# Kernel tuning notes

Hardware: AMD Instinct MI355X
Metric: run time of the kernel (lower is better)

The kernel has to match this reference:

```python
import jax, jax.numpy as jnp
import numpy as np

KS = 3
N = KS * KS
LN_EPS = 1e-5


def conv2d(x, w, stride=1, pad=0):
    return jax.lax.conv_general_dilated(
        x, w, (stride, stride), [(pad, pad), (pad, pad)],
        dimension_numbers=('NCHW', 'OIHW', 'NCHW'))


def layer_norm(x, g, b):
    mu = jnp.mean(x, axis=-1, keepdims=True)
    var = jnp.mean(jnp.square(x - mu), axis=-1, keepdims=True)
    return (x - mu) * jax.lax.rsqrt(var + LN_EPS) * g + b


def l2norm(x):
    n = jnp.sqrt(jnp.sum(jnp.square(x), axis=-1, keepdims=True))
    return x / jnp.maximum(n, 1e-12)


def deform_conv(x, w_p, b_p, w_d):
    # canonical DeformConv2d (kernel 3, pad 1, stride 1, no modulation)
    B, C, H, W = x.shape
    off = conv2d(x, w_p, stride=1, pad=1) + b_p[None, :, None, None]  # [B,2N,H,W]
    xp = jnp.pad(x, ((0, 0), (0, 0), (1, 1), (1, 1)))
    Hp, Wp = H + 2, W + 2
    pn = jnp.stack(jnp.meshgrid(jnp.arange(-1, 2), jnp.arange(-1, 2), indexing='ij'), 0)
    pn = pn.reshape(2, N).astype(x.dtype)  # kernel offsets, row-major (dx,dy)
    p0x = jnp.arange(1, H + 1, dtype=x.dtype)
    p0y = jnp.arange(1, W + 1, dtype=x.dtype)
    # sampling coords, [B,H,W,N]
    px = off[:, :N].transpose(0, 2, 3, 1) + p0x[None, :, None, None] + pn[0][None, None, None, :]
    py = off[:, N:].transpose(0, 2, 3, 1) + p0y[None, None, :, None] + pn[1][None, None, None, :]
    fx = jnp.floor(px)
    fy = jnp.floor(py)
    qlx = jnp.clip(fx, 0, Hp - 1)
    qly = jnp.clip(fy, 0, Wp - 1)
    qrx = jnp.clip(fx + 1, 0, Hp - 1)
    qry = jnp.clip(fy + 1, 0, Wp - 1)
    pxc = jnp.clip(px, 0, Hp - 1)
    pyc = jnp.clip(py, 0, Wp - 1)
    g_lt = (1 + (qlx - pxc)) * (1 + (qly - pyc))
    g_rb = (1 - (qrx - pxc)) * (1 - (qry - pyc))
    g_lb = (1 + (qlx - pxc)) * (1 - (qry - pyc))
    g_rt = (1 - (qrx - pxc)) * (1 + (qly - pyc))
    xf = xp.reshape(B, C, Hp * Wp)

    def gat(ix, iy):
        idx = (ix.astype(jnp.int32) * Wp + iy.astype(jnp.int32)).reshape(B, 1, -1)
        g = jnp.take_along_axis(xf, jnp.broadcast_to(idx, (B, C, idx.shape[-1])), axis=2)
        return g.reshape(B, C, H, W, N)

    xo = (g_lt[:, None] * gat(qlx, qly) + g_rb[:, None] * gat(qrx, qry)
          + g_lb[:, None] * gat(qlx, qry) + g_rt[:, None] * gat(qrx, qly))
    # [B,C,H,W,N] -> [B,C,H*ks,W*ks] (row = h*ks+kr, col = w*ks+kc)
    xo = xo.reshape(B, C, H, W, KS, KS).transpose(0, 1, 2, 4, 3, 5).reshape(B, C, H * KS, W * KS)
    return conv2d(xo, w_d, stride=KS, pad=0)


def setup_inputs() -> dict:
    key = jax.random.key(0)
    ks = jax.random.split(key, 8)
    B, C, H, W, heads = 4, 192, 64, 64, 6
    hid = 4 * C
    return {
        'x': jax.random.normal(ks[0], (B, C, H, W), dtype=jnp.float32),
        'gamma1': jnp.ones((C,), jnp.float32),
        'beta1': jnp.zeros((C,), jnp.float32),
        'gamma2': jnp.ones((C,), jnp.float32),
        'beta2': jnp.zeros((C,), jnp.float32),
        'temperature': jnp.ones((heads, 1, 1), jnp.float32),
        'w_qkv': jax.random.normal(ks[1], (3 * C, C), jnp.float32) * 0.02,
        'w_proj': jax.random.normal(ks[2], (C, C), jnp.float32) * 0.02,
        'w_p': jax.random.normal(ks[3], (2 * N, C, KS, KS), jnp.float32) * 0.01,
        'b_p': jnp.zeros((2 * N,), jnp.float32),
        'w_d': jax.random.normal(ks[4], (C, C, KS, KS), jnp.float32) * 0.02,
        'w_fc1': jax.random.normal(ks[5], (C, hid), jnp.float32) * 0.02,
        'b_fc1': jnp.zeros((hid,), jnp.float32),
        'w_fc2': jax.random.normal(ks[6], (hid, C), jnp.float32) * 0.02,
        'b_fc2': jnp.zeros((C,), jnp.float32),
    }


def reference(x, gamma1, beta1, gamma2, beta2, temperature, w_qkv, w_proj,
              w_p, b_p, w_d, w_fc1, b_fc1, w_fc2, b_fc2):
    B, C, H, W = x.shape
    heads = temperature.shape[0]
    xs = x.reshape(B, C, H * W).transpose(0, 2, 1)  # [B,HW,C]
    shortcut = xs
    xn = layer_norm(xs, gamma1, beta1).transpose(0, 2, 1).reshape(B, C, H, W)
    # SSA: deformable-conv query + channel attention over C
    q = deform_conv(xn, w_p, b_p, w_d)
    qkv = jnp.einsum('bchw,oc->bohw', xn, w_qkv)
    k_spe, v_spe = qkv[:, C:2 * C], qkv[:, 2 * C:]

    def split(t):
        return t.reshape(B, heads, C // heads, H * W)

    qh = split(q)
    kh = l2norm(split(k_spe))
    vh = l2norm(split(v_spe))
    attn = jnp.einsum('bhcn,bhdn->bhcd', qh, kh) * temperature[None]
    attn = jax.nn.softmax(attn, axis=-1)
    out = jnp.einsum('bhcd,bhdn->bhcn', attn, vh).reshape(B, C, H, W)
    out = jnp.einsum('bchw,oc->bohw', out, w_proj)
    xs2 = shortcut + out.reshape(B, C, H * W).transpose(0, 2, 1)
    h1 = layer_norm(xs2, gamma2, beta2)
    m = jax.nn.gelu(h1 @ w_fc1 + b_fc1, approximate=False) @ w_fc2 + b_fc2
    xs3 = xs2 + m
    return xs3.transpose(0, 2, 1).reshape(B, C, H, W)
```

## Files before the change

kernel.cpp:

```cpp
#include <hip/hip_runtime.h>
#include <math.h>

typedef unsigned short u16;
typedef unsigned int u32;
typedef short s16x8 __attribute__((ext_vector_type(8)));
typedef float f32x4 __attribute__((ext_vector_type(4)));

#define AS1 __attribute__((address_space(1)))
#define AS3 __attribute__((address_space(3)))

__device__ __forceinline__ float bf2f(u16 u) {
    union { u32 i; float f; } v; v.i = ((u32)u) << 16; return v.f;
}
__device__ __forceinline__ u16 f2bf(float f) {
    union { float f; u32 i; } v; v.f = f;
    u32 r = v.i + 0x7fffu + ((v.i >> 16) & 1u);
    return (u16)(r >> 16);
}
__device__ __forceinline__ void gll16(const u16* g, u16* l) {
    __builtin_amdgcn_global_load_lds((const AS1 u32*)g, (AS3 u32*)l, 16, 0, 0);
}

__global__ void prep_kernel(const float* __restrict__ wd, const float* __restrict__ wqkv,
                            const float* __restrict__ wfc1, const float* __restrict__ wfc2,
                            const float* __restrict__ wp,
                            u16* __restrict__ wdT, u16* __restrict__ wkvT,
                            u16* __restrict__ wf1T, u16* __restrict__ wf2T,
                            u16* __restrict__ wpT)
{
    int i = blockIdx.x * 256 + threadIdx.x;
    if (i < 331776) {
        int o = i / 1728, r = i % 1728;
        int p = r / 192, c = r % 192;
        int cs = c ^ ((o & 7) << 3);
        wdT[(p * 192 + o) * 192 + cs] = f2bf(wd[(o * 192 + c) * 9 + p]);
    }
    if (i < 73728) {
        int o = i / 192, c = i % 192;
        wkvT[i] = f2bf(wqkv[(192 + o) * 192 + c]);
    }
    if (i < 147456) {
        int n = i / 192, c = i % 192;
        wf1T[i] = f2bf(wfc1[c * 768 + n]);
        int n2 = i / 768, hh = i % 768;
        wf2T[i] = f2bf(wfc2[hh * 192 + n2]);
    }
    if (i < 31104) {
        int n = i / 1728, r = i % 1728;
        int p = r / 192, c = r % 192;
        wpT[i] = f2bf(wp[(n * 192 + c) * 9 + p]);
    } else if (i < 55296) {
        wpT[i] = 0;
    }
}

__global__ __launch_bounds__(256) void ln1_kernel(const float* __restrict__ x,
                                                  const float* __restrict__ g,
                                                  const float* __restrict__ be,
                                                  u16* __restrict__ xn)
{
    __shared__ float red0[256], red1[256];
    __shared__ float mu_s[64], rs_s[64];
    __shared__ float xt[64 * 193];
    __shared__ u16 tile[64 * 194];
    int t = threadIdx.x, tl = t & 63, cg = t >> 6;
    int m0 = blockIdx.x * 64;
    int b = m0 >> 12, hw0 = m0 & 4095;
    const float* xb = x + (size_t)b * 786432 + hw0 + tl;
    float s = 0.f, s2 = 0.f;
    for (int cc = cg; cc < 192; cc += 4) {
        float v = xb[cc * 4096];
        xt[tl * 193 + cc] = v;
        s += v; s2 += v * v;
    }
    red0[t] = s; red1[t] = s2;
    __syncthreads();
    if (t < 64) {
        float a = red0[t] + red0[64 + t] + red0[128 + t] + red0[192 + t];
        float q = red1[t] + red1[64 + t] + red1[128 + t] + red1[192 + t];
        float mu = a * (1.f / 192.f);
        float var = q * (1.f / 192.f) - mu * mu;
        mu_s[t] = mu; rs_s[t] = rsqrtf(var + 1e-5f);
    }
    __syncthreads();
    float mu = mu_s[tl], rs = rs_s[tl];
    for (int cc = cg; cc < 192; cc += 4) {
        float v = (xt[tl * 193 + cc] - mu) * rs * g[cc] + be[cc];
        tile[tl * 194 + cc] = f2bf(v);
    }
    __syncthreads();
    u32* dst = (u32*)(xn + (size_t)m0 * 192);
    for (int i = t; i < 64 * 96; i += 256) {
        int r = i / 96, c2 = i % 96;
        dst[i] = *(const u32*)&tile[r * 194 + c2 * 2];
    }
}

__global__ __launch_bounds__(256) void offconv_kernel(const u16* __restrict__ xn,
                                                      const u16* __restrict__ wpT,
                                                      const float* __restrict__ bp,
                                                      float* __restrict__ off)
{
    __shared__ u16 As[64 * 200];
    __shared__ u16 Bs[32 * 200];
    int bh = blockIdx.x;
    int b = bh >> 6, h = bh & 63;
    int t = threadIdx.x;
    int lane = t & 63, wv = t >> 6;
    f32x4 acc[2];
#pragma unroll
    for (int j = 0; j < 2; j++) { acc[j][0] = 0.f; acc[j][1] = 0.f; acc[j][2] = 0.f; acc[j][3] = 0.f; }
    int r = t >> 2, cq = (t & 3) * 48;
    for (int p = 0; p < 9; p++) {
        int dh = p / 3 - 1, dw = p % 3 - 1;
        int hr = h + dh, wr = r + dw;
        bool valid = (hr >= 0) && (hr < 64) && (wr >= 0) && (wr < 64);
        const u16* src = xn + ((size_t)(b * 4096 + hr * 64 + wr)) * 192 + cq;
#pragma unroll
        for (int j = 0; j < 6; j++) {
            s16x8 v = {0, 0, 0, 0, 0, 0, 0, 0};
            if (valid) v = *(const s16x8*)(src + j * 8);
            *(s16x8*)&As[r * 200 + cq + j * 8] = v;
        }
#pragma unroll
        for (int i = 0; i < 3; i++) {
            int q = t + i * 256;
            int n = q / 24, c8 = q % 24;
            *(s16x8*)&Bs[n * 200 + c8 * 8] =
                *(const s16x8*)(wpT + n * 1728 + p * 192 + c8 * 8);
        }
        __syncthreads();
#pragma unroll
        for (int kc = 0; kc < 6; kc++) {
            s16x8 af = *(const s16x8*)&As[(wv * 16 + (lane & 15)) * 200 + kc * 32 + (lane >> 4) * 8];
            s16x8 b0 = *(const s16x8*)&Bs[(lane & 15) * 200 + kc * 32 + (lane >> 4) * 8];
            s16x8 b1 = *(const s16x8*)&Bs[(16 + (lane & 15)) * 200 + kc * 32 + (lane >> 4) * 8];
            acc[0] = __builtin_amdgcn_mfma_f32_16x16x32_bf16(af, b0, acc[0], 0, 0, 0);
            acc[1] = __builtin_amdgcn_mfma_f32_16x16x32_bf16(af, b1, acc[1], 0, 0, 0);
        }
        __syncthreads();
    }
    int col = lane & 15;
    int wbase = wv * 16 + (lane >> 4) * 4;
#pragma unroll
    for (int j = 0; j < 2; j++) {
        int n = j * 16 + col;
        if (n < 18) {
            float bb = bp[n];
#pragma unroll
            for (int rr = 0; rr < 4; rr++) {
                int w = wbase + rr;
                off[((size_t)(b * 4096 + h * 64 + w)) * 18 + n] = acc[j][rr] + bb;
            }
        }
    }
}

__global__ __launch_bounds__(512, 2) void gemm_deform(const u16* __restrict__ xn,
                                                      const float* __restrict__ off,
                                                      const u16* __restrict__ wdT,
                                                      u16* __restrict__ qt)
{
    __shared__ u16 As[64 * 200];
    __shared__ u16 Bs[192 * 192];
    __shared__ int sidx[64][9][4];
    __shared__ float swt[64][9][4];
    int t = threadIdx.x, lane = t & 63, wv = t >> 6;
    int wm = wv & 1, wn = wv >> 1;
    int m0 = blockIdx.x * 64;
    int b = m0 >> 12;
    for (int i = t; i < 576; i += 512) {
        int mi = i / 9, p = i % 9;
        int m = m0 + mi;
        int hw = m & 4095;
        int h = hw >> 6, w = hw & 63;
        float ox = off[(size_t)m * 18 + p];
        float oy = off[(size_t)m * 18 + 9 + p];
        float px = ox + (float)(h + 1) + (float)(p / 3 - 1);
        float py = oy + (float)(w + 1) + (float)(p % 3 - 1);
        float fx = floorf(px), fy = floorf(py);
        float qlx = fminf(fmaxf(fx, 0.f), 65.f);
        float qly = fminf(fmaxf(fy, 0.f), 65.f);
        float qrx = fminf(fmaxf(fx + 1.f, 0.f), 65.f);
        float qry = fminf(fmaxf(fy + 1.f, 0.f), 65.f);
        float pxc = fminf(fmaxf(px, 0.f), 65.f);
        float pyc = fminf(fmaxf(py, 0.f), 65.f);
        float gxl = 1.f + (qlx - pxc), gxr = 1.f - (qrx - pxc);
        float gyl = 1.f + (qly - pyc), gyr = 1.f - (qry - pyc);
        int xl = (int)qlx, xr = (int)qrx, yl = (int)qly, yr = (int)qry;
        int cx[4] = {xl, xr, xl, xr};
        int cy[4] = {yl, yr, yr, yl};
        float cw[4] = {gxl * gyl, gxr * gyr, gxl * gyr, gxr * gyl};
#pragma unroll
        for (int k = 0; k < 4; k++) {
            bool ok = (cx[k] >= 1) && (cx[k] <= 64) && (cy[k] >= 1) && (cy[k] <= 64);
            sidx[mi][p][k] = ok ? (b * 4096 + (cx[k] - 1) * 64 + (cy[k] - 1)) * 192 : 0;
            swt[mi][p][k] = ok ? cw[k] : 0.f;
        }
    }
    __syncthreads();
    f32x4 acc[2][3];
#pragma unroll
    for (int i = 0; i < 2; i++)
#pragma unroll
        for (int j = 0; j < 3; j++) {
            acc[i][j][0] = 0.f; acc[i][j][1] = 0.f; acc[i][j][2] = 0.f; acc[i][j][3] = 0.f;
        }
    int mi = t >> 3, ch = (t & 7) * 24;
    int orow[3], oxr[3];
#pragma unroll
    for (int j = 0; j < 3; j++) {
        int o = wn * 48 + j * 16 + (lane & 15);
        orow[j] = o * 192;
        oxr[j] = (o & 7) << 3;
    }
    int kb0 = (lane >> 4) * 8;

    {
        const u16* bsrc = wdT;
#pragma unroll
        for (int i2 = 0; i2 < 9; i2++) {
            int jc = wv + 8 * i2;
            gll16(bsrc + jc * 512 + lane * 8, Bs + jc * 512);
        }
        const int*   si = sidx[mi][0];
        const float* sw = swt[mi][0];
        s16x8 pc[4][3];
#pragma unroll
        for (int k = 0; k < 4; k++)
#pragma unroll
            for (int s = 0; s < 3; s++)
                pc[k][s] = *(const s16x8*)(xn + si[k] + ch + s * 8);
        float v[24];
#pragma unroll
        for (int j = 0; j < 24; j++) v[j] = 0.f;
#pragma unroll
        for (int k = 0; k < 4; k++) {
            float wt = sw[k];
#pragma unroll
            for (int j = 0; j < 24; j++) v[j] += wt * bf2f((u16)pc[k][j >> 3][j & 7]);
        }
#pragma unroll
        for (int s = 0; s < 3; s++) {
            s16x8 ov;
#pragma unroll
            for (int e = 0; e < 8; e++) ov[e] = (short)f2bf(v[s * 8 + e]);
            *(s16x8*)&As[mi * 200 + ch + s * 8] = ov;
        }
        asm volatile("s_waitcnt vmcnt(0)" ::: "memory");
        __syncthreads();
    }

    for (int p = 0; p < 9; p++) {
        s16x8 nc[4][3];
        if (p < 8) {
            const int* si = sidx[mi][p + 1];
#pragma unroll
            for (int k = 0; k < 4; k++)
#pragma unroll
                for (int s = 0; s < 3; s++)
                    nc[k][s] = *(const s16x8*)(xn + si[k] + ch + s * 8);
        }
#pragma unroll
        for (int kk = 0; kk < 6; kk++) {
            int kb = kk * 32 + kb0;
            s16x8 af[2], bfr[3];
#pragma unroll
            for (int i = 0; i < 2; i++)
                af[i] = *(const s16x8*)&As[(wm * 32 + i * 16 + (lane & 15)) * 200 + kb];
#pragma unroll
            for (int j = 0; j < 3; j++)
                bfr[j] = *(const s16x8*)&Bs[orow[j] + (kb ^ oxr[j])];
#pragma unroll
            for (int i = 0; i < 2; i++)
#pragma unroll
                for (int j = 0; j < 3; j++)
                    acc[i][j] = __builtin_amdgcn_mfma_f32_16x16x32_bf16(af[i], bfr[j], acc[i][j], 0, 0, 0);
        }
        if (p < 8) {
            __syncthreads();
            const u16* bsrc = wdT + (size_t)(p + 1) * 36864;
#pragma unroll
            for (int i2 = 0; i2 < 9; i2++) {
                int jc = wv + 8 * i2;
                gll16(bsrc + jc * 512 + lane * 8, Bs + jc * 512);
            }
            const float* sw = swt[mi][p + 1];
            float v[24];
#pragma unroll
            for (int j = 0; j < 24; j++) v[j] = 0.f;
#pragma unroll
            for (int k = 0; k < 4; k++) {
                float wt = sw[k];
#pragma unroll
                for (int j = 0; j < 24; j++) v[j] += wt * bf2f((u16)nc[k][j >> 3][j & 7]);
            }
#pragma unroll
            for (int s = 0; s < 3; s++) {
                s16x8 ov;
#pragma unroll
                for (int e = 0; e < 8; e++) ov[e] = (short)f2bf(v[s * 8 + e]);
                *(s16x8*)&As[mi * 200 + ch + s * 8] = ov;
            }
            asm volatile("s_waitcnt vmcnt(0)" ::: "memory");
            __syncthreads();
        }
    }
    int col = lane & 15;
#pragma unroll
    for (int i = 0; i < 2; i++)
#pragma unroll
        for (int j = 0; j < 3; j++) {
            int mm = m0 + wm * 32 + i * 16 + (lane >> 4) * 4;
            int nn = wn * 48 + j * 16 + col;
#pragma unroll
            for (int r = 0; r < 4; r++)
                qt[(size_t)(mm + r) * 192 + nn] = f2bf(acc[i][j][r]);
        }
}

template<int BM, int BN, int WM, int WN, int EP>
__global__ __launch_bounds__((BM / WM) * (BN / WN) * 64)
void gemm_bt(const u16* __restrict__ A, int lda,
             const u16* __restrict__ B, int ldb, int bstride,
             void* __restrict__ out, int ldc,
             const float* __restrict__ ex1, int K,
             const float* __restrict__ ex2,
             const float* __restrict__ exg, const float* __restrict__ exb,
             void* __restrict__ out2)
{
    constexpr int BK = 32;
    constexpr int WAVES_M = BM / WM, WAVES_N = BN / WN, NW = WAVES_M * WAVES_N;
    constexpr int TM = WM / 16, TN = WN / 16;
    constexpr int NLA = BM / 16, NLB = BN / 16;
    __shared__ u16 As[BM * BK];
    __shared__ u16 Bs[BN * BK];
    int tid = threadIdx.x;
    int lane = tid & 63, wv = tid >> 6;
    int wm = wv % WAVES_M, wn = wv / WAVES_M;
    int m0 = blockIdx.x * BM, n0 = blockIdx.y * BN;
    const u16* Bp = B + (size_t)(m0 >> 12) * bstride;
    f32x4 acc[TM][TN];
#pragma unroll
    for (int i = 0; i < TM; i++)
#pragma unroll
        for (int j = 0; j < TN; j++) {
            acc[i][j][0] = 0.f; acc[i][j][1] = 0.f; acc[i][j][2] = 0.f; acc[i][j][3] = 0.f;
        }
    int arow_l = lane >> 2;
    int acol_l = (lane & 3) * 8;
    for (int k0 = 0; k0 < K; k0 += BK) {
#pragma unroll 1
        for (int j = wv; j < NLA + NLB; j += NW) {
            if (j < NLA) {
                int row = j * 16 + arow_l;
                gll16(A + (size_t)(m0 + row) * lda + k0 + acol_l, As + j * 512);
            } else {
                int row = (j - NLA) * 16 + arow_l;
                gll16(Bp + (size_t)(n0 + row) * ldb + k0 + acol_l, Bs + (j - NLA) * 512);
            }
        }
        asm volatile("s_waitcnt vmcnt(0)" ::: "memory");
        __syncthreads();
        s16x8 af[TM], bfr[TN];
#pragma unroll
        for (int i = 0; i < TM; i++)
            af[i] = *(const s16x8*)&As[(wm * WM + i * 16 + (lane & 15)) * BK + (lane >> 4) * 8];
#pragma unroll
        for (int j = 0; j < TN; j++)
            bfr[j] = *(const s16x8*)&Bs[(wn * WN + j * 16 + (lane & 15)) * BK + (lane >> 4) * 8];
#pragma unroll
        for (int i = 0; i < TM; i++)
#pragma unroll
            for (int j = 0; j < TN; j++)
                acc[i][j] = __builtin_amdgcn_mfma_f32_16x16x32_bf16(af[i], bfr[j], acc[i][j], 0, 0, 0);
        __syncthreads();
    }
    int col = lane & 15;
    int rg = lane >> 4;
    if constexpr (EP == 2) {
        u16* o = (u16*)out;
#pragma unroll
        for (int i = 0; i < TM; i++)
#pragma unroll
            for (int j = 0; j < TN; j++) {
                int mm = m0 + wm * WM + i * 16 + rg * 4;
                int nn = n0 + wn * WN + j * 16 + col;
                float bb = ex1[nn];
#pragma unroll
                for (int r = 0; r < 4; r++) {
                    float v = acc[i][j][r] + bb;
                    o[(size_t)(mm + r) * ldc + nn] = f2bf(0.5f * v * (1.f + erff(v * 0.70710678118654752f)));
                }
            }
    } else if constexpr (EP == 4) {
        __shared__ float lnA[BM][WAVES_N];
        __shared__ float lnB[BM][WAVES_N];
        float v[TM][TN][4];
        float sr[TM][4], sq[TM][4];
#pragma unroll
        for (int i = 0; i < TM; i++)
#pragma unroll
            for (int r = 0; r < 4; r++) { sr[i][r] = 0.f; sq[i][r] = 0.f; }
#pragma unroll
        for (int i = 0; i < TM; i++) {
            int mm = m0 + wm * WM + i * 16 + rg * 4;
#pragma unroll
            for (int j = 0; j < TN; j++) {
                int nn = n0 + wn * WN + j * 16 + col;
                const float* xr = ex1 + (size_t)(mm >> 12) * 786432 + (size_t)nn * 4096 + (mm & 4095);
#pragma unroll
                for (int r = 0; r < 4; r++) {
                    float vv = acc[i][j][r] + xr[r];
                    v[i][j][r] = vv;
                    sr[i][r] += vv; sq[i][r] += vv * vv;
                }
            }
        }
#pragma unroll
        for (int i = 0; i < TM; i++)
#pragma unroll
            for (int r = 0; r < 4; r++)
#pragma unroll
                for (int sh = 1; sh < 16; sh <<= 1) {
                    sr[i][r] += __shfl_xor(sr[i][r], sh);
                    sq[i][r] += __shfl_xor(sq[i][r], sh);
                }
        if (col == 0) {
#pragma unroll
            for (int i = 0; i < TM; i++)
#pragma unroll
                for (int r = 0; r < 4; r++) {
                    int row = wm * WM + i * 16 + rg * 4 + r;
                    lnA[row][wn] = sr[i][r];
                    lnB[row][wn] = sq[i][r];
                }
        }
        __syncthreads();
        float* oxs = (float*)out;
        u16* oh = (u16*)out2;
#pragma unroll
        for (int i = 0; i < TM; i++) {
            int mm = m0 + wm * WM + i * 16 + rg * 4;
#pragma unroll
            for (int r = 0; r < 4; r++) {
                int row = wm * WM + i * 16 + rg * 4 + r;
                float tot = 0.f, tq = 0.f;
#pragma unroll
                for (int q2 = 0; q2 < WAVES_N; q2++) { tot += lnA[row][q2]; tq += lnB[row][q2]; }
                float mu = tot * (1.f / 192.f);
                float var = tq * (1.f / 192.f) - mu * mu;
                float rstd = rsqrtf(var + 1e-5f);
#pragma unroll
                for (int j = 0; j < TN; j++) {
                    int nn = n0 + wn * WN + j * 16 + col;
                    float vv = v[i][j][r];
                    oxs[(size_t)(mm + r) * ldc + nn] = vv;
                    oh[(size_t)(mm + r) * ldc + nn] = f2bf((vv - mu) * rstd * exg[nn] + exb[nn]);
                }
            }
        }
    } else if constexpr (EP == 5) {
        float* o = (float*)out;
#pragma unroll
        for (int i = 0; i < TM; i++)
#pragma unroll
            for (int j = 0; j < TN; j++) {
                int mm = m0 + wm * WM + i * 16 + rg * 4;
                int nn = n0 + wn * WN + j * 16 + col;
                float bb = ex1[nn];
                size_t obase = (size_t)(mm >> 12) * 786432 + (size_t)nn * 4096;
#pragma unroll
                for (int r = 0; r < 4; r++) {
                    float vv = acc[i][j][r] + bb + ex2[(size_t)(mm + r) * ldc + nn];
                    o[obase + ((mm + r) & 4095)] = vv;
                }
            }
    } else if constexpr (EP == 6) {
        u16* o = (u16*)out;
        float* nrm = (float*)out2;
        int bI = m0 >> 12;
#pragma unroll
        for (int j = 0; j < TN; j++) {
            float s = 0.f;
#pragma unroll
            for (int i = 0; i < TM; i++) {
                int mm = m0 + wm * WM + i * 16 + rg * 4;
                int nn = n0 + wn * WN + j * 16 + col;
#pragma unroll
                for (int r = 0; r < 4; r++) {
                    u16 hb = f2bf(acc[i][j][r]);
                    o[(size_t)(mm + r) * ldc + nn] = hb;
                    float fv = bf2f(hb);
                    s += fv * fv;
                }
            }
            s += __shfl_xor(s, 16);
            s += __shfl_xor(s, 32);
            if (rg == 0) {
                int nn = n0 + wn * WN + j * 16 + col;
                atomicAdd(&nrm[bI * 384 + nn], s);
            }
        }
    }
}

__global__ __launch_bounds__(64) void attnp_kernel(const u16* __restrict__ qt,
                                                   const u16* __restrict__ kvt,
                                                   float* __restrict__ raw)
{
    __shared__ float qT[32 * 69];
    __shared__ float kT[32 * 69];
    int ch = blockIdx.x, h = blockIdx.y, b = blockIdx.z;
    int t = threadIdx.x;
    size_t base = (size_t)(b * 4096 + ch * 64);
    for (int e = t; e < 2048; e += 64) {
        int r = e >> 5, c = e & 31;
        qT[c * 69 + r] = bf2f(qt[(base + r) * 192 + h * 32 + c]);
        kT[c * 69 + r] = bf2f(kvt[(base + r) * 384 + h * 32 + c]);
    }
    __syncthreads();
    int tc = t >> 3, td = t & 7;
    int c0 = tc * 4, d0 = td * 4;
    float acc[4][4] = {};
    for (int r = 0; r < 64; r++) {
        float qv[4], kv4[4];
#pragma unroll
        for (int u = 0; u < 4; u++) { qv[u] = qT[(c0 + u) * 69 + r]; kv4[u] = kT[(d0 + u) * 69 + r]; }
#pragma unroll
        for (int u = 0; u < 4; u++)
#pragma unroll
            for (int v = 0; v < 4; v++) acc[u][v] += qv[u] * kv4[v];
    }
    float* dst = raw + (((size_t)(b * 6 + h) * 64 + ch) * 1024);
#pragma unroll
    for (int u = 0; u < 4; u++)
#pragma unroll
        for (int v = 0; v < 4; v++)
            dst[(c0 + u) * 32 + d0 + v] = acc[u][v];
}

__global__ __launch_bounds__(1024) void softmax_kernel(const float* __restrict__ raw,
                                                       const float* __restrict__ norm2,
                                                       const float* __restrict__ temp,
                                                       float* __restrict__ att2)
{
    int h = blockIdx.x, b = blockIdx.y;
    int t = threadIdx.x;
    int c = t >> 5, d = t & 31;
    __shared__ float invk[32], invv[32];
    if (t < 32)       invk[t] = 1.f / fmaxf(sqrtf(norm2[b * 384 + h * 32 + t]), 1e-12f);
    else if (t < 64)  invv[t - 32] = 1.f / fmaxf(sqrtf(norm2[b * 384 + 192 + h * 32 + (t - 32)]), 1e-12f);
    __syncthreads();
    float T = temp[h];
    const float* pr = raw + (size_t)(b * 6 + h) * 65536 + c * 32 + d;
    float v = 0.f;
#pragma unroll
    for (int ch = 0; ch < 64; ch++) v += pr[ch * 1024];
    v *= invk[d] * T;
    float mx = v;
    for (int s = 16; s > 0; s >>= 1) mx = fmaxf(mx, __shfl_xor(mx, s, 32));
    float e = expf(v - mx);
    float sm = e;
    for (int s = 16; s > 0; s >>= 1) sm += __shfl_xor(sm, s, 32);
    att2[((size_t)(b * 6 + h) * 32 + c) * 32 + d] = (e / sm) * invv[d];
}

__global__ __launch_bounds__(192) void mb_kernel(const float* __restrict__ wproj,
                                                 const float* __restrict__ att2,
                                                 u16* __restrict__ Mb)
{
    int o2 = blockIdx.x, b = blockIdx.y, t = threadIdx.x;
    int h = t >> 5, d = t & 31;
    float s = 0.f;
#pragma unroll
    for (int c = 0; c < 32; c++)
        s += wproj[o2 * 192 + h * 32 + c] * att2[((size_t)(b * 6 + h) * 32 + c) * 32 + d];
    Mb[((size_t)b * 192 + o2) * 192 + t] = f2bf(s);
}

extern "C" void kernel_launch(void* const* d_in, const int* in_sizes, int n_in,
                              void* d_out, int out_size, void* d_ws, size_t ws_size,
                              hipStream_t stream)
{
    const float* x      = (const float*)d_in[0];
    const float* gamma1 = (const float*)d_in[1];
    const float* beta1  = (const float*)d_in[2];
    const float* gamma2 = (const float*)d_in[3];
    const float* beta2  = (const float*)d_in[4];
    const float* temp   = (const float*)d_in[5];
    const float* w_qkv  = (const float*)d_in[6];
    const float* w_proj = (const float*)d_in[7];
    const float* w_p    = (const float*)d_in[8];
    const float* b_p    = (const float*)d_in[9];
    const float* w_d    = (const float*)d_in[10];
    const float* w_fc1  = (const float*)d_in[11];
    const float* b_fc1  = (const float*)d_in[12];
    const float* w_fc2  = (const float*)d_in[13];
    const float* b_fc2  = (const float*)d_in[14];
    float* out = (float*)d_out;
    char* ws = (char*)d_ws;

    u16*   xn    = (u16*)(ws + 0);
    float* off   = (float*)(ws + 6291456);
    u16*   adef  = (u16*)(ws + 7471104);
    u16*   wpT   = adef;
    u16*   m1    = adef;
    float* araw  = (float*)(ws + 32636928);
    u16*   qt    = (u16*)(ws + 64094208);
    u16*   kvt   = (u16*)(ws + 70385664);
    float* norm2 = (float*)(ws + 82968576);
    float* att2  = (float*)(ws + 83073024);
    u16*   Mb    = (u16*)(ws + 83171328);
    float* xs2   = (float*)(ws + 83318784);
    u16*   h1    = xn;
    u16*   wdT   = (u16*)(ws + 95901696);
    u16*   wkvT  = (u16*)(ws + 96565248);
    u16*   wf1T  = (u16*)(ws + 96712704);
    u16*   wf2T  = (u16*)(ws + 97007616);

    hipMemsetAsync(norm2, 0, 6144, stream);
    prep_kernel<<<1296, 256, 0, stream>>>(w_d, w_qkv, w_fc1, w_fc2, w_p, wdT, wkvT, wf1T, wf2T, wpT);
    ln1_kernel<<<256, 256, 0, stream>>>(x, gamma1, beta1, xn);
    offconv_kernel<<<256, 256, 0, stream>>>(xn, wpT, b_p, off);
    gemm_deform<<<256, 512, 0, stream>>>(xn, off, wdT, qt);
    gemm_bt<128, 128, 64, 64, 6><<<dim3(128, 3), 256, 0, stream>>>(
        xn, 192, wkvT, 192, 0, kvt, 384, nullptr, 192, nullptr, nullptr, nullptr, norm2);
    attnp_kernel<<<dim3(64, 6, 4), 64, 0, stream>>>(qt, kvt, araw);
    softmax_kernel<<<dim3(6, 4), 1024, 0, stream>>>(araw, norm2, temp, att2);
    mb_kernel<<<dim3(192, 4), 192, 0, stream>>>(w_proj, att2, Mb);
    gemm_bt<64, 192, 32, 48, 4><<<dim3(256, 1), 512, 0, stream>>>(
        kvt + 192, 384, Mb, 192, 192 * 192, xs2, 192, x, 192, nullptr, gamma2, beta2, h1);
    gemm_bt<128, 128, 64, 64, 2><<<dim3(128, 6), 256, 0, stream>>>(
        h1, 192, wf1T, 192, 0, m1, 768, b_fc1, 192, nullptr, nullptr, nullptr, nullptr);
    gemm_bt<128, 96, 32, 48, 5><<<dim3(128, 2), 512, 0, stream>>>(
        m1, 768, wf2T, 768, 0, out, 192, b_fc2, 768, xs2, nullptr, nullptr, nullptr);
}
```

Baseline: 241.9 us.

## Fuse softmax with projection-matrix build, fold memset into prep, widen offconv and attnp loads

```diff
diff --git a/kernel.cpp b/kernel.cpp
--- a/kernel.cpp
+++ b/kernel.cpp
@@ -26,9 +26,10 @@
                             const float* __restrict__ wp,
                             u16* __restrict__ wdT, u16* __restrict__ wkvT,
                             u16* __restrict__ wf1T, u16* __restrict__ wf2T,
-                            u16* __restrict__ wpT)
+                            u16* __restrict__ wpT, float* __restrict__ norm2)
 {
     int i = blockIdx.x * 256 + threadIdx.x;
+    if (i < 1536) norm2[i] = 0.f;
     if (i < 331776) {
         int o = i / 1728, r = i % 1728;
         int p = r / 192, c = r % 192;
@@ -96,7 +97,7 @@
     }
 }
 
-__global__ __launch_bounds__(256) void offconv_kernel(const u16* __restrict__ xn,
+__global__ __launch_bounds__(512) void offconv_kernel(const u16* __restrict__ xn,
                                                       const u16* __restrict__ wpT,
                                                       const float* __restrict__ bp,
                                                       float* __restrict__ off)
@@ -107,51 +108,48 @@
     int b = bh >> 6, h = bh & 63;
     int t = threadIdx.x;
     int lane = t & 63, wv = t >> 6;
-    f32x4 acc[2];
-#pragma unroll
-    for (int j = 0; j < 2; j++) { acc[j][0] = 0.f; acc[j][1] = 0.f; acc[j][2] = 0.f; acc[j][3] = 0.f; }
-    int r = t >> 2, cq = (t & 3) * 48;
+    int wm = wv & 3, wn = wv >> 2;
+    f32x4 acc;
+    acc[0] = 0.f; acc[1] = 0.f; acc[2] = 0.f; acc[3] = 0.f;
+    int r = t >> 3, cq = (t & 7) * 24;
     for (int p = 0; p < 9; p++) {
         int dh = p / 3 - 1, dw = p % 3 - 1;
         int hr = h + dh, wr = r + dw;
         bool valid = (hr >= 0) && (hr < 64) && (wr >= 0) && (wr < 64);
         const u16* src = xn + ((size_t)(b * 4096 + hr * 64 + wr)) * 192 + cq;
 #pragma unroll
-        for (int j = 0; j < 6; j++) {
+        for (int j = 0; j < 3; j++) {
             s16x8 v = {0, 0, 0, 0, 0, 0, 0, 0};
             if (valid) v = *(const s16x8*)(src + j * 8);
             *(s16x8*)&As[r * 200 + cq + j * 8] = v;
         }
 #pragma unroll
-        for (int i = 0; i < 3; i++) {
-            int q = t + i * 256;
-            int n = q / 24, c8 = q % 24;
-            *(s16x8*)&Bs[n * 200 + c8 * 8] =
-                *(const s16x8*)(wpT + n * 1728 + p * 192 + c8 * 8);
+        for (int i = 0; i < 2; i++) {
+            int q = t + i * 512;
+            if (q < 768) {
+                int n = q / 24, c8 = q % 24;
+                *(s16x8*)&Bs[n * 200 + c8 * 8] =
+                    *(const s16x8*)(wpT + n * 1728 + p * 192 + c8 * 8);
+            }
         }
         __syncthreads();
 #pragma unroll
         for (int kc = 0; kc < 6; kc++) {
-            s16x8 af = *(const s16x8*)&As[(wv * 16 + (lane & 15)) * 200 + kc * 32 + (lane >> 4) * 8];
-            s16x8 b0 = *(const s16x8*)&Bs[(lane & 15) * 200 + kc * 32 + (lane >> 4) * 8];
-            s16x8 b1 = *(const s16x8*)&Bs[(16 + (lane & 15)) * 200 + kc * 32 + (lane >> 4) * 8];
-            acc[0] = __builtin_amdgcn_mfma_f32_16x16x32_bf16(af, b0, acc[0], 0, 0, 0);
-            acc[1] = __builtin_amdgcn_mfma_f32_16x16x32_bf16(af, b1, acc[1], 0, 0, 0);
+            s16x8 af = *(const s16x8*)&As[(wm * 16 + (lane & 15)) * 200 + kc * 32 + (lane >> 4) * 8];
+            s16x8 b0 = *(const s16x8*)&Bs[(wn * 16 + (lane & 15)) * 200 + kc * 32 + (lane >> 4) * 8];
+            acc = __builtin_amdgcn_mfma_f32_16x16x32_bf16(af, b0, acc, 0, 0, 0);
         }
         __syncthreads();
     }
     int col = lane & 15;
-    int wbase = wv * 16 + (lane >> 4) * 4;
-#pragma unroll
-    for (int j = 0; j < 2; j++) {
-        int n = j * 16 + col;
-        if (n < 18) {
-            float bb = bp[n];
-#pragma unroll
-            for (int rr = 0; rr < 4; rr++) {
-                int w = wbase + rr;
-                off[((size_t)(b * 4096 + h * 64 + w)) * 18 + n] = acc[j][rr] + bb;
-            }
+    int n = wn * 16 + col;
+    int wbase = wm * 16 + (lane >> 4) * 4;
+    if (n < 18) {
+        float bb = bp[n];
+#pragma unroll
+        for (int rr = 0; rr < 4; rr++) {
+            int w = wbase + rr;
+            off[((size_t)(b * 4096 + h * 64 + w)) * 18 + n] = acc[rr] + bb;
         }
     }
 }
@@ -514,10 +512,17 @@
     int ch = blockIdx.x, h = blockIdx.y, b = blockIdx.z;
     int t = threadIdx.x;
     size_t base = (size_t)(b * 4096 + ch * 64);
-    for (int e = t; e < 2048; e += 64) {
-        int r = e >> 5, c = e & 31;
-        qT[c * 69 + r] = bf2f(qt[(base + r) * 192 + h * 32 + c]);
-        kT[c * 69 + r] = bf2f(kvt[(base + r) * 384 + h * 32 + c]);
+#pragma unroll
+    for (int i = 0; i < 4; i++) {
+        int e = t + i * 64;
+        int r = e >> 2, c8 = (e & 3) * 8;
+        s16x8 qv = *(const s16x8*)(qt + (base + r) * 192 + h * 32 + c8);
+        s16x8 kv = *(const s16x8*)(kvt + (base + r) * 384 + h * 32 + c8);
+#pragma unroll
+        for (int j = 0; j < 8; j++) {
+            qT[(c8 + j) * 69 + r] = bf2f((u16)qv[j]);
+            kT[(c8 + j) * 69 + r] = bf2f((u16)kv[j]);
+        }
     }
     __syncthreads();
     int tc = t >> 3, td = t & 7;
@@ -540,15 +545,17 @@
             dst[(c0 + u) * 32 + d0 + v] = acc[u][v];
 }
 
-__global__ __launch_bounds__(1024) void softmax_kernel(const float* __restrict__ raw,
+__global__ __launch_bounds__(1024) void attnfin_kernel(const float* __restrict__ raw,
                                                        const float* __restrict__ norm2,
                                                        const float* __restrict__ temp,
-                                                       float* __restrict__ att2)
+                                                       const float* __restrict__ wproj,
+                                                       u16* __restrict__ Mb)
 {
     int h = blockIdx.x, b = blockIdx.y;
     int t = threadIdx.x;
     int c = t >> 5, d = t & 31;
     __shared__ float invk[32], invv[32];
+    __shared__ float attL[32][33];
     if (t < 32)       invk[t] = 1.f / fmaxf(sqrtf(norm2[b * 384 + h * 32 + t]), 1e-12f);
     else if (t < 64)  invv[t - 32] = 1.f / fmaxf(sqrtf(norm2[b * 384 + 192 + h * 32 + (t - 32)]), 1e-12f);
     __syncthreads();
@@ -563,20 +570,18 @@
     float e = expf(v - mx);
     float sm = e;
     for (int s = 16; s > 0; s >>= 1) sm += __shfl_xor(sm, s, 32);
-    att2[((size_t)(b * 6 + h) * 32 + c) * 32 + d] = (e / sm) * invv[d];
-}
-
-__global__ __launch_bounds__(192) void mb_kernel(const float* __restrict__ wproj,
-                                                 const float* __restrict__ att2,
-                                                 u16* __restrict__ Mb)
-{
-    int o2 = blockIdx.x, b = blockIdx.y, t = threadIdx.x;
-    int h = t >> 5, d = t & 31;
-    float s = 0.f;
-#pragma unroll
-    for (int c = 0; c < 32; c++)
-        s += wproj[o2 * 192 + h * 32 + c] * att2[((size_t)(b * 6 + h) * 32 + c) * 32 + d];
-    Mb[((size_t)b * 192 + o2) * 192 + t] = f2bf(s);
+    attL[c][d] = (e / sm) * invv[d];
+    __syncthreads();
+#pragma unroll
+    for (int i2 = 0; i2 < 6; i2++) {
+        int i = t + i2 * 1024;
+        int o2 = i >> 5, dd = i & 31;
+        float s = 0.f;
+#pragma unroll
+        for (int c2 = 0; c2 < 32; c2++)
+            s += wproj[o2 * 192 + h * 32 + c2] * attL[c2][dd];
+        Mb[((size_t)b * 192 + o2) * 192 + h * 32 + dd] = f2bf(s);
+    }
 }
 
 extern "C" void kernel_launch(void* const* d_in, const int* in_sizes, int n_in,
@@ -610,7 +615,6 @@
     u16*   qt    = (u16*)(ws + 64094208);
     u16*   kvt   = (u16*)(ws + 70385664);
     float* norm2 = (float*)(ws + 82968576);
-    float* att2  = (float*)(ws + 83073024);
     u16*   Mb    = (u16*)(ws + 83171328);
     float* xs2   = (float*)(ws + 83318784);
     u16*   h1    = xn;
@@ -619,16 +623,14 @@
     u16*   wf1T  = (u16*)(ws + 96712704);
     u16*   wf2T  = (u16*)(ws + 97007616);
 
-    hipMemsetAsync(norm2, 0, 6144, stream);
-    prep_kernel<<<1296, 256, 0, stream>>>(w_d, w_qkv, w_fc1, w_fc2, w_p, wdT, wkvT, wf1T, wf2T, wpT);
+    prep_kernel<<<1296, 256, 0, stream>>>(w_d, w_qkv, w_fc1, w_fc2, w_p, wdT, wkvT, wf1T, wf2T, wpT, norm2);
     ln1_kernel<<<256, 256, 0, stream>>>(x, gamma1, beta1, xn);
-    offconv_kernel<<<256, 256, 0, stream>>>(xn, wpT, b_p, off);
+    offconv_kernel<<<256, 512, 0, stream>>>(xn, wpT, b_p, off);
     gemm_deform<<<256, 512, 0, stream>>>(xn, off, wdT, qt);
     gemm_bt<128, 128, 64, 64, 6><<<dim3(128, 3), 256, 0, stream>>>(
         xn, 192, wkvT, 192, 0, kvt, 384, nullptr, 192, nullptr, nullptr, nullptr, norm2);
     attnp_kernel<<<dim3(64, 6, 4), 64, 0, stream>>>(qt, kvt, araw);
-    softmax_kernel<<<dim3(6, 4), 1024, 0, stream>>>(araw, norm2, temp, att2);
-    mb_kernel<<<dim3(192, 4), 192, 0, stream>>>(w_proj, att2, Mb);
+    attnfin_kernel<<<dim3(6, 4), 1024, 0, stream>>>(araw, norm2, temp, w_proj, Mb);
     gemm_bt<64, 192, 32, 48, 4><<<dim3(256, 1), 512, 0, stream>>>(
         kvt + 192, 384, Mb, 192, 192 * 192, xs2, 192, x, 192, nullptr, gamma2, beta2, h1);
     gemm_bt<128, 128, 64, 64, 2><<<dim3(128, 6), 256, 0, stream>>>(
```

Result: no change. 241.1 us (-0.3%).
